# Kernel optimization log

Measured on AMD Instinct MI355X. Metric: run time of the kernel, lower is better.

## Reference

```python
import jax, jax.numpy as jnp
import numpy as np

NUM_SEGMENTS = 16

def setup_inputs() -> dict:
    key = jax.random.key(0)
    k1, k2, k3, k4 = jax.random.split(key, 4)
    C, R = 256, 4
    x = jax.random.normal(k1, (1000000, C), dtype=jnp.float32)
    indices = jax.random.randint(k2, (1000000,), 0, NUM_SEGMENTS, dtype=jnp.int64)
    # Linear weights (torch Linear: y = x @ W.T); store as (in, out) for einsum
    w1 = jax.random.normal(k3, (C, C // R), dtype=jnp.float32) / np.sqrt(C)
    w2 = jax.random.normal(k4, (C // R, C), dtype=jnp.float32) / np.sqrt(C // R)
    return {"x": x, "indices": indices, "w1": w1, "w2": w2}

def reference(x, indices, w1, w2):
    idx = indices.astype(jnp.int32)
    # scatter-mean over segments: (S, C)
    seg_sum = jax.ops.segment_sum(x, idx, num_segments=NUM_SEGMENTS)
    counts = jax.ops.segment_sum(jnp.ones((x.shape[0],), x.dtype), idx, num_segments=NUM_SEGMENTS)
    seg_mean = seg_sum / jnp.maximum(counts, 1.0)[:, None]
    # tiny SE MLP: Linear -> ReLU -> Linear -> Sigmoid
    h = jax.nn.relu(seg_mean @ w1)
    gate = jax.nn.sigmoid(h @ w2)  # (S, C)
    # gather per-point gate and modulate
    return x * gate[idx]
```

## Files before the change

kernel.cpp:

```cpp
#include <hip/hip_runtime.h>
#include <math.h>

#define C 256
#define S 16
#define CR 64
#define NREP 16

typedef float f4 __attribute__((ext_vector_type(4)));

__global__ __launch_bounds__(256) void k_hist(
    const int* __restrict__ idx, int* __restrict__ pcnt, int nrows)
{
    const int lane = threadIdx.x & 63;
    const int tid  = blockIdx.x * blockDim.x + threadIdx.x;
    const int T    = gridDim.x * blockDim.x;
    const int padded = ((nrows + 63) >> 6) << 6;

    int c0=0,c1=0,c2=0,c3=0,c4=0,c5=0,c6=0,c7=0,
        c8=0,c9=0,c10=0,c11=0,c12=0,c13=0,c14=0,c15=0;

    for (int i = tid; i < padded; i += T) {
        const int v = (i < nrows) ? idx[i] : -1;
        #define CNT(K) c##K += (int)__popcll(__ballot(v == K));
        CNT(0)  CNT(1)  CNT(2)  CNT(3)  CNT(4)  CNT(5)  CNT(6)  CNT(7)
        CNT(8)  CNT(9)  CNT(10) CNT(11) CNT(12) CNT(13) CNT(14) CNT(15)
        #undef CNT
    }
    if (lane == 0) {
        #define FL(K) if (c##K) atomicAdd(&pcnt[K], c##K);
        FL(0)  FL(1)  FL(2)  FL(3)  FL(4)  FL(5)  FL(6)  FL(7)
        FL(8)  FL(9)  FL(10) FL(11) FL(12) FL(13) FL(14) FL(15)
        #undef FL
    }
}

__global__ __launch_bounds__(256, 4) void k_segsum(
    const float* __restrict__ x, const int* __restrict__ idx,
    float* __restrict__ psum, int nrows)
{
    const int  tid = blockIdx.x * 256 + threadIdx.x;
    const int  T   = gridDim.x * 256;
    const long n4  = (long)nrows * (C / 4);

    f4 a0={0,0,0,0},a1={0,0,0,0},a2={0,0,0,0},a3={0,0,0,0},
       a4={0,0,0,0},a5={0,0,0,0},a6={0,0,0,0},a7={0,0,0,0},
       a8={0,0,0,0},a9={0,0,0,0},a10={0,0,0,0},a11={0,0,0,0},
       a12={0,0,0,0},a13={0,0,0,0},a14={0,0,0,0},a15={0,0,0,0};

    const f4* __restrict__ x4 = reinterpret_cast<const f4*>(x);

    #define ACC1(K, sv, vv) { const float m = (sv == K) ? 1.0f : 0.0f; \
        a##K.x = fmaf(m, vv.x, a##K.x); a##K.y = fmaf(m, vv.y, a##K.y); \
        a##K.z = fmaf(m, vv.z, a##K.z); a##K.w = fmaf(m, vv.w, a##K.w); }
    #define ROW(sv, vv) \
        ACC1(0,sv,vv)  ACC1(1,sv,vv)  ACC1(2,sv,vv)  ACC1(3,sv,vv) \
        ACC1(4,sv,vv)  ACC1(5,sv,vv)  ACC1(6,sv,vv)  ACC1(7,sv,vv) \
        ACC1(8,sv,vv)  ACC1(9,sv,vv)  ACC1(10,sv,vv) ACC1(11,sv,vv) \
        ACC1(12,sv,vv) ACC1(13,sv,vv) ACC1(14,sv,vv) ACC1(15,sv,vv)

    long i = tid;
    for (; i + T < n4; i += 2L * T) {
        const f4  v0 = x4[i];
        const f4  v1 = x4[i + T];
        const int s0 = idx[i >> 6];
        const int s1 = idx[(i + T) >> 6];
        ROW(s0, v0)
        ROW(s1, v1)
    }
    for (; i < n4; i += T) {
        const f4  v = x4[i];
        const int s = idx[i >> 6];
        ROW(s, v)
    }
    #undef ROW
    #undef ACC1

    __shared__ float red[4][8][C];
    const int w    = threadIdx.x >> 6;
    const int lane = threadIdx.x & 63;
    const int t    = threadIdx.x;
    const int rep  = blockIdx.x & (NREP - 1);
    float* gs = psum + (size_t)rep * S * C;

    #define ST(K, SL) *reinterpret_cast<f4*>(&red[w][SL][4 * lane]) = a##K;
    ST(0,0) ST(1,1) ST(2,2) ST(3,3) ST(4,4) ST(5,5) ST(6,6) ST(7,7)
    __syncthreads();
    #pragma unroll
    for (int s_ = 0; s_ < 8; s_++) {
        const float v = red[0][s_][t] + red[1][s_][t] +
                        red[2][s_][t] + red[3][s_][t];
        atomicAdd(&gs[s_ * C + t], v);
    }
    __syncthreads();
    ST(8,0) ST(9,1) ST(10,2) ST(11,3) ST(12,4) ST(13,5) ST(14,6) ST(15,7)
    __syncthreads();
    #pragma unroll
    for (int s_ = 0; s_ < 8; s_++) {
        const float v = red[0][s_][t] + red[1][s_][t] +
                        red[2][s_][t] + red[3][s_][t];
        atomicAdd(&gs[(8 + s_) * C + t], v);
    }
    #undef ST
}

__global__ __launch_bounds__(256) void k_mlp(
    const float* __restrict__ psum, const int* __restrict__ pcnt,
    const float* __restrict__ w1, const float* __restrict__ w2,
    float* __restrict__ gate)
{
    __shared__ float sm[S][C];
    __shared__ float h[S][CR];
    __shared__ float cnt[S];
    const int t = threadIdx.x;

    if (t < S) cnt[t] = fmaxf((float)pcnt[t], 1.0f);
    __syncthreads();

    for (int i = t; i < S * C; i += 256) {
        float v = 0.0f;
        #pragma unroll
        for (int r = 0; r < NREP; r++) v += psum[r * S * C + i];
        sm[i / C][i % C] = v / cnt[i / C];
    }
    __syncthreads();

    for (int o = t; o < S * CR; o += 256) {
        const int s = o / CR, j = o % CR;
        float acc = 0.0f;
        #pragma unroll 4
        for (int k = 0; k < C; k++) acc += sm[s][k] * w1[k * CR + j];
        h[s][j] = fmaxf(acc, 0.0f);
    }
    __syncthreads();

    for (int o = t; o < S * C; o += 256) {
        const int s = o / C, j = o % C;
        float acc = 0.0f;
        #pragma unroll
        for (int k = 0; k < CR; k++) acc += h[s][k] * w2[k * C + j];
        gate[o] = 1.0f / (1.0f + expf(-acc));
    }
}

__global__ __launch_bounds__(256) void k_mod(
    const float* __restrict__ x, const int* __restrict__ idx,
    const float* __restrict__ gate, float* __restrict__ out, int nrows)
{
    const int l    = threadIdx.x & 63;
    const int wrow = threadIdx.x >> 6;
    const float4* __restrict__ x4 = reinterpret_cast<const float4*>(x);
    const float4* __restrict__ g4 = reinterpret_cast<const float4*>(gate);
    float4* __restrict__ o4 = reinterpret_cast<float4*>(out);

    for (int row = blockIdx.x * 4 + wrow; row < nrows; row += gridDim.x * 4) {
        const int s = idx[row];
        float4 v = x4[row * (C / 4) + l];
        const float4 g = g4[s * (C / 4) + l];
        v.x *= g.x; v.y *= g.y; v.z *= g.z; v.w *= g.w;
        o4[row * (C / 4) + l] = v;
    }
}

extern "C" void kernel_launch(void* const* d_in, const int* in_sizes, int n_in,
                              void* d_out, int out_size, void* d_ws, size_t ws_size,
                              hipStream_t stream)
{
    const float* x   = (const float*)d_in[0];
    const int*   idx = (const int*)  d_in[1];
    const float* w1  = (const float*)d_in[2];
    const float* w2  = (const float*)d_in[3];
    float* out = (float*)d_out;
    const int nrows = in_sizes[1];

    float* psum = (float*)d_ws;
    int*   pcnt = (int*)(psum + NREP * S * C);
    float* gate = (float*)(pcnt + S);

    const size_t zero_bytes = NREP * S * C * sizeof(float) + S * sizeof(int);
    (void)hipMemsetAsync(d_ws, 0, zero_bytes, stream);

    k_hist  <<< 128, 256, 0, stream>>>(idx, pcnt, nrows);
    k_segsum<<<1024, 256, 0, stream>>>(x, idx, psum, nrows);
    k_mlp   <<<   1, 256, 0, stream>>>(psum, pcnt, w1, w2, gate);
    k_mod   <<<2048, 256, 0, stream>>>(x, idx, gate, out, nrows);
}
```

Measured before the change: 794.3 us.

## Restructure segment-sum into row superblocks with per-block partials and parallel MLP

The segment-sum kernel now processes 64-row superblocks, loading the index once per lane and broadcasting it with readlane. Each block batches eight vector loads before accumulating, and writes its partial sums to its own slot instead of atomically adding into 16 replicas. The MLP kernel runs one block per segment and reduces all block partials in parallel, which drops the large memset. The modulate kernel walks rows in reverse, presumably to reuse recently cached x, and uses nontemporal stores for the output. The cost is a larger workspace and a bigger partial-reduction read in the MLP stage.

```diff
diff --git a/kernel.cpp b/kernel.cpp
--- a/kernel.cpp
+++ b/kernel.cpp
@@ -4,7 +4,6 @@
 #define C 256
 #define S 16
 #define CR 64
-#define NREP 16
 
 typedef float f4 __attribute__((ext_vector_type(4)));
 
@@ -36,11 +35,10 @@
 
 __global__ __launch_bounds__(256, 4) void k_segsum(
     const float* __restrict__ x, const int* __restrict__ idx,
-    float* __restrict__ psum, int nrows)
+    float* __restrict__ parts, int nrows)
 {
-    const int  tid = blockIdx.x * 256 + threadIdx.x;
-    const int  T   = gridDim.x * 256;
-    const long n4  = (long)nrows * (C / 4);
+    const int lane = threadIdx.x & 63;
+    const int w    = threadIdx.x >> 6;
 
     f4 a0={0,0,0,0},a1={0,0,0,0},a2={0,0,0,0},a3={0,0,0,0},
        a4={0,0,0,0},a5={0,0,0,0},a6={0,0,0,0},a7={0,0,0,0},
@@ -58,88 +56,91 @@
         ACC1(8,sv,vv)  ACC1(9,sv,vv)  ACC1(10,sv,vv) ACC1(11,sv,vv) \
         ACC1(12,sv,vv) ACC1(13,sv,vv) ACC1(14,sv,vv) ACC1(15,sv,vv)
 
-    long i = tid;
-    for (; i + T < n4; i += 2L * T) {
-        const f4  v0 = x4[i];
-        const f4  v1 = x4[i + T];
-        const int s0 = idx[i >> 6];
-        const int s1 = idx[(i + T) >> 6];
-        ROW(s0, v0)
-        ROW(s1, v1)
+    const int nsb = nrows >> 6;
+    for (int sb = blockIdx.x; sb < nsb; sb += gridDim.x) {
+        const int row0 = sb << 6;
+        const int vidx = idx[row0 + lane];
+        const f4* __restrict__ p = x4 + (size_t)(row0 + (w << 4)) * (C/4) + lane;
+        #pragma unroll 1
+        for (int j = 0; j < 16; j += 8) {
+            f4  v[8];
+            int s[8];
+            #pragma unroll
+            for (int k = 0; k < 8; k++)
+                v[k] = p[(size_t)(j + k) * (C/4)];
+            #pragma unroll
+            for (int k = 0; k < 8; k++)
+                s[k] = __builtin_amdgcn_readlane(vidx, (w << 4) + j + k);
+            #pragma unroll
+            for (int k = 0; k < 8; k++) { ROW(s[k], v[k]) }
+        }
     }
-    for (; i < n4; i += T) {
-        const f4  v = x4[i];
-        const int s = idx[i >> 6];
-        ROW(s, v)
+    if (blockIdx.x == 0 && w == 0) {
+        for (int r = nsb << 6; r < nrows; ++r) {
+            const int sv = __builtin_amdgcn_readfirstlane(idx[r]);
+            const f4 vv = x4[(size_t)r * (C/4) + lane];
+            ROW(sv, vv)
+        }
     }
     #undef ROW
     #undef ACC1
 
     __shared__ float red[4][8][C];
-    const int w    = threadIdx.x >> 6;
-    const int lane = threadIdx.x & 63;
-    const int t    = threadIdx.x;
-    const int rep  = blockIdx.x & (NREP - 1);
-    float* gs = psum + (size_t)rep * S * C;
+    const int t = threadIdx.x;
+    float* slot = parts + (size_t)blockIdx.x * S * C;
 
     #define ST(K, SL) *reinterpret_cast<f4*>(&red[w][SL][4 * lane]) = a##K;
     ST(0,0) ST(1,1) ST(2,2) ST(3,3) ST(4,4) ST(5,5) ST(6,6) ST(7,7)
     __syncthreads();
     #pragma unroll
-    for (int s_ = 0; s_ < 8; s_++) {
-        const float v = red[0][s_][t] + red[1][s_][t] +
-                        red[2][s_][t] + red[3][s_][t];
-        atomicAdd(&gs[s_ * C + t], v);
-    }
+    for (int s_ = 0; s_ < 8; s_++)
+        slot[s_ * C + t] = red[0][s_][t] + red[1][s_][t] +
+                           red[2][s_][t] + red[3][s_][t];
     __syncthreads();
     ST(8,0) ST(9,1) ST(10,2) ST(11,3) ST(12,4) ST(13,5) ST(14,6) ST(15,7)
     __syncthreads();
     #pragma unroll
-    for (int s_ = 0; s_ < 8; s_++) {
-        const float v = red[0][s_][t] + red[1][s_][t] +
-                        red[2][s_][t] + red[3][s_][t];
-        atomicAdd(&gs[(8 + s_) * C + t], v);
-    }
+    for (int s_ = 0; s_ < 8; s_++)
+        slot[(8 + s_) * C + t] = red[0][s_][t] + red[1][s_][t] +
+                                 red[2][s_][t] + red[3][s_][t];
     #undef ST
 }
 
 __global__ __launch_bounds__(256) void k_mlp(
-    const float* __restrict__ psum, const int* __restrict__ pcnt,
+    const float* __restrict__ parts, const int* __restrict__ pcnt,
     const float* __restrict__ w1, const float* __restrict__ w2,
-    float* __restrict__ gate)
+    float* __restrict__ gate, int nparts)
 {
-    __shared__ float sm[S][C];
-    __shared__ float h[S][CR];
-    __shared__ float cnt[S];
+    __shared__ float sm[C];
+    __shared__ float h[CR];
+    const int b = blockIdx.x;
     const int t = threadIdx.x;
 
-    if (t < S) cnt[t] = fmaxf((float)pcnt[t], 1.0f);
+    float r0 = 0, r1 = 0, r2 = 0, r3 = 0;
+    int p = 0;
+    for (; p + 4 <= nparts; p += 4) {
+        r0 += parts[(size_t)(p+0) * S * C + b * C + t];
+        r1 += parts[(size_t)(p+1) * S * C + b * C + t];
+        r2 += parts[(size_t)(p+2) * S * C + b * C + t];
+        r3 += parts[(size_t)(p+3) * S * C + b * C + t];
+    }
+    for (; p < nparts; p++) r0 += parts[(size_t)p * S * C + b * C + t];
+    const float cnt = fmaxf((float)pcnt[b], 1.0f);
+    sm[t] = ((r0 + r1) + (r2 + r3)) / cnt;
     __syncthreads();
 
-    for (int i = t; i < S * C; i += 256) {
-        float v = 0.0f;
-        #pragma unroll
-        for (int r = 0; r < NREP; r++) v += psum[r * S * C + i];
-        sm[i / C][i % C] = v / cnt[i / C];
+    if (t < CR) {
+        float acc = 0.0f;
+        #pragma unroll 4
+        for (int k = 0; k < C; k++) acc += sm[k] * w1[k * CR + t];
+        h[t] = fmaxf(acc, 0.0f);
     }
     __syncthreads();
 
-    for (int o = t; o < S * CR; o += 256) {
-        const int s = o / CR, j = o % CR;
-        float acc = 0.0f;
-        #pragma unroll 4
-        for (int k = 0; k < C; k++) acc += sm[s][k] * w1[k * CR + j];
-        h[s][j] = fmaxf(acc, 0.0f);
-    }
-    __syncthreads();
-
-    for (int o = t; o < S * C; o += 256) {
-        const int s = o / C, j = o % C;
-        float acc = 0.0f;
-        #pragma unroll
-        for (int k = 0; k < CR; k++) acc += h[s][k] * w2[k * C + j];
-        gate[o] = 1.0f / (1.0f + expf(-acc));
-    }
+    float acc = 0.0f;
+    #pragma unroll
+    for (int k = 0; k < CR; k++) acc += h[k] * w2[k * C + t];
+    gate[b * C + t] = 1.0f / (1.0f + expf(-acc));
 }
 
 __global__ __launch_bounds__(256) void k_mod(
@@ -148,16 +149,17 @@
 {
     const int l    = threadIdx.x & 63;
     const int wrow = threadIdx.x >> 6;
-    const float4* __restrict__ x4 = reinterpret_cast<const float4*>(x);
-    const float4* __restrict__ g4 = reinterpret_cast<const float4*>(gate);
-    float4* __restrict__ o4 = reinterpret_cast<float4*>(out);
+    const f4* __restrict__ x4 = reinterpret_cast<const f4*>(x);
+    const f4* __restrict__ g4 = reinterpret_cast<const f4*>(gate);
+    f4* __restrict__ o4 = reinterpret_cast<f4*>(out);
 
-    for (int row = blockIdx.x * 4 + wrow; row < nrows; row += gridDim.x * 4) {
+    for (int r = blockIdx.x * 4 + wrow; r < nrows; r += gridDim.x * 4) {
+        const int row = nrows - 1 - r;
         const int s = idx[row];
-        float4 v = x4[row * (C / 4) + l];
-        const float4 g = g4[s * (C / 4) + l];
-        v.x *= g.x; v.y *= g.y; v.z *= g.z; v.w *= g.w;
-        o4[row * (C / 4) + l] = v;
+        f4 v = x4[(size_t)row * (C/4) + l];
+        const f4 g = g4[s * (C/4) + l];
+        v *= g;
+        __builtin_nontemporal_store(v, &o4[(size_t)row * (C/4) + l]);
     }
 }
 
@@ -172,15 +174,18 @@
     float* out = (float*)d_out;
     const int nrows = in_sizes[1];
 
-    float* psum = (float*)d_ws;
-    int*   pcnt = (int*)(psum + NREP * S * C);
-    float* gate = (float*)(pcnt + S);
+    const size_t fixed = S * sizeof(int) + S * C * sizeof(float);
+    int sgrid = 1024;
+    if (ws_size < (size_t)sgrid * S * C * sizeof(float) + fixed) sgrid = 256;
 
-    const size_t zero_bytes = NREP * S * C * sizeof(float) + S * sizeof(int);
-    (void)hipMemsetAsync(d_ws, 0, zero_bytes, stream);
+    float* parts = (float*)d_ws;
+    int*   pcnt  = (int*)(parts + (size_t)sgrid * S * C);
+    float* gate  = (float*)(pcnt + S);
 
-    k_hist  <<< 128, 256, 0, stream>>>(idx, pcnt, nrows);
-    k_segsum<<<1024, 256, 0, stream>>>(x, idx, psum, nrows);
-    k_mlp   <<<   1, 256, 0, stream>>>(psum, pcnt, w1, w2, gate);
-    k_mod   <<<2048, 256, 0, stream>>>(x, idx, gate, out, nrows);
+    (void)hipMemsetAsync(pcnt, 0, S * sizeof(int), stream);
+
+    k_hist  <<<  128, 256, 0, stream>>>(idx, pcnt, nrows);
+    k_segsum<<<sgrid, 256, 0, stream>>>(x, idx, parts, nrows);
+    k_mlp   <<<    S, 256, 0, stream>>>(parts, pcnt, w1, w2, gate, sgrid);
+    k_mod   <<< 2048, 256, 0, stream>>>(x, idx, gate, out, nrows);
 }
```

New measurement: 777.4 us. 2.1% less time.
